# Kernel tuning notes

Measured on AMD Instinct MI355X. Metric: run time of the kernel, lower is better.

The kernel has to match this reference:

```python
import jax, jax.numpy as jnp
import numpy as np

N, D, K, E_T = 16384, 64, 3, 262144
EPS = 1e-8

def layernorm(x, g, b):
    m = x.mean(-1, keepdims=True)
    v = x.var(-1, keepdims=True)
    return (x - m) * jax.lax.rsqrt(v + 1e-5) * g + b

def knn_edges(coords, k):
    # PyG knn_graph(loop=False, flow='source_to_target'): edge (neighbor -> query)
    n = coords.shape[0]
    sq = jnp.sum(coords * coords, axis=-1)
    d = sq[:, None] + sq[None, :] - 2.0 * (coords @ coords.T)  # [N,N] sq dists
    d = d.at[jnp.arange(n), jnp.arange(n)].set(jnp.inf)  # exclude self
    _, idx = jax.lax.top_k(-d, k)  # [N,k] nearest neighbor indices
    src = idx.reshape(-1)
    dst = jnp.repeat(jnp.arange(n), k)
    return src, dst

def gcn_conv(x, W, b, src, dst, ew, n):
    h = x @ W
    deg = jax.ops.segment_sum(ew, dst, num_segments=n)
    dis = jnp.where(deg > 0, jax.lax.rsqrt(jnp.maximum(deg, EPS)), 0.0)
    norm = dis[src] * ew * dis[dst]
    out = jax.ops.segment_sum(h[src] * norm[:, None], dst, num_segments=n)
    return out + b

def setup_inputs():
    key = jax.random.key(0)
    ks = jax.random.split(key, 8)
    return {
        "sp_center_feat": jax.random.normal(ks[0], (N, D), jnp.float32),
        "edge_index_tran": jax.random.randint(ks[1], (2, E_T), 0, N),
        "edge_attr_rpe": jax.random.normal(ks[2], (E_T, 3), jnp.float32),
        "norm_index": jax.random.randint(ks[3], (2,), 0, N),
        "sp_crood": jax.random.uniform(ks[4], (N, 3), jnp.float32),
        "norm1_g": jnp.ones((D,), jnp.float32), "norm1_b": jnp.zeros((D,), jnp.float32),
        "norm2_g": jnp.ones((D,), jnp.float32), "norm2_b": jnp.zeros((D,), jnp.float32),
        "gcn_norm_g": jnp.ones((D,), jnp.float32), "gcn_norm_b": jnp.zeros((D,), jnp.float32),
        "W1": jax.random.normal(ks[5], (D, D), jnp.float32) / np.sqrt(D),
        "b1": jnp.zeros((D,), jnp.float32),
        "W2": jax.random.normal(ks[6], (D, D), jnp.float32) / np.sqrt(D),
        "b2": jnp.zeros((D,), jnp.float32),
    }

def reference(sp_center_feat, edge_index_tran, edge_attr_rpe, norm_index, sp_crood,
              norm1_g, norm1_b, norm2_g, norm2_b, gcn_norm_g, gcn_norm_b,
              W1, b1, W2, b2):
    n = sp_center_feat.shape[0]
    x = layernorm(sp_center_feat, norm1_g, norm1_b)
    x = x + x  # SPgrah (external transformer) stubbed as identity; module adds shortcut
    x = layernorm(x, norm2_g, norm2_b)
    shortcut = x
    src, dst = knn_edges(sp_crood, K)
    a = x[src]; b_ = x[dst]
    na = jnp.maximum(jnp.sqrt(jnp.sum(a * a, -1)), EPS)
    nb = jnp.maximum(jnp.sqrt(jnp.sum(b_ * b_, -1)), EPS)
    ew_knn = jax.nn.sigmoid(jnp.sum(a * b_, -1) / (na * nb))  # sigmoid(cosine sim)
    loop = jnp.arange(n)
    src2 = jnp.concatenate([src, loop])
    dst2 = jnp.concatenate([dst, loop])
    ew = jnp.concatenate([ew_knn, jnp.ones((n,), ew_knn.dtype)])  # self-loops w=1
    h = gcn_conv(x, W1, b1, src2, dst2, ew, n)
    h = jax.nn.relu(layernorm(h, gcn_norm_g, gcn_norm_b))
    h = gcn_conv(h, W2, b2, src2, dst2, ew, n)
    h = h + x  # residual inside SuperpointGCN
    return shortcut + h
```

## Files before the change

### kernel.cpp

```cpp
#include <hip/hip_runtime.h>
#include <math.h>

#define N 16384
#define GC 8
#define NCELL (GC*GC*GC)

__device__ __forceinline__ float wsum(float v){
  #pragma unroll
  for(int m=32;m>0;m>>=1) v += __shfl_xor(v,m,64);
  return v;
}

__device__ __forceinline__ void lexins(float dd,int j2,
    float&D0,float&D1,float&D2,int&I0,int&I1,int&I2){
  bool lt0=(dd<D0)||((dd==D0)&&(j2<I0));
  bool lt1=(dd<D1)||((dd==D1)&&(j2<I1));
  bool lt2=(dd<D2)||((dd==D2)&&(j2<I2));
  float nD2=lt1?D1:(lt2?dd:D2); int nI2=lt1?I1:(lt2?j2:I2);
  float nD1=lt0?D0:(lt1?dd:D1); int nI1=lt0?I0:(lt1?j2:I1);
  float nD0=lt0?dd:D0;          int nI0=lt0?j2:I0;
  D0=nD0;D1=nD1;D2=nD2;I0=nI0;I1=nI1;I2=nI2;
}

__device__ __forceinline__ float refdist(float qx,float qy,float qz,float qs,float4 cv){
  float dot=__fmaf_rn(qz,cv.z,__fmaf_rn(qy,cv.y,__fmul_rn(qx,cv.x)));
  float sc =__fadd_rn(qs,cv.w);
  return __fmaf_rn(-2.0f,dot,sc);
}

__global__ __launch_bounds__(256) void ln_kernel(const float* __restrict__ in,
    const float* __restrict__ g1,const float* __restrict__ b1,
    const float* __restrict__ g2,const float* __restrict__ b2,
    const float* __restrict__ coords,
    float* __restrict__ x, float* __restrict__ xn, float4* __restrict__ c4){
  int wave=threadIdx.x>>6, lane=threadIdx.x&63;
  int row=blockIdx.x*4+wave;
  float v=in[row*64+lane];
  float m=wsum(v)*(1.0f/64.0f);
  float d=v-m;
  float var=wsum(d*d)*(1.0f/64.0f);
  float y=d*(1.0f/sqrtf(var+1e-5f))*g1[lane]+b1[lane];
  y=y+y;
  float m2=wsum(y)*(1.0f/64.0f);
  float d2=y-m2;
  float var2=wsum(d2*d2)*(1.0f/64.0f);
  float z=d2*(1.0f/sqrtf(var2+1e-5f))*g2[lane]+b2[lane];
  x[row*64+lane]=z;
  float s=wsum(z*z);
  if(lane==0){
    xn[row]=fmaxf(sqrtf(s),1e-8f);
    float a=coords[row*3+0],b=coords[row*3+1],c=coords[row*3+2];
    float sq=__fadd_rn(__fadd_rn(__fmul_rn(a,a),__fmul_rn(b,b)),__fmul_rn(c,c));
    c4[row]=make_float4(a,b,c,sq);
  }
}

__global__ __launch_bounds__(1024) void prep(const float4* __restrict__ c4,
    float4* __restrict__ sc4, int* __restrict__ sidx, int* __restrict__ cellSt){
  __shared__ int cnt[NCELL];
  __shared__ int scanbuf[NCELL];
  int tid=threadIdx.x;
  if(tid<NCELL) cnt[tid]=0;
  __syncthreads();
  for(int i=tid;i<N;i+=1024){
    float4 v=c4[i];
    int cx=min(GC-1,(int)(v.x*(float)GC)), cy=min(GC-1,(int)(v.y*(float)GC)),
        cz=min(GC-1,(int)(v.z*(float)GC));
    atomicAdd(&cnt[(cz*GC+cy)*GC+cx],1);
  }
  __syncthreads();
  if(tid<NCELL) scanbuf[tid]=cnt[tid];
  __syncthreads();
  for(int off=1;off<NCELL;off<<=1){
    int t=0;
    if(tid>=off && tid<NCELL) t=scanbuf[tid-off];
    __syncthreads();
    if(tid<NCELL) scanbuf[tid]+=t;
    __syncthreads();
  }
  if(tid<NCELL){
    int excl=scanbuf[tid]-cnt[tid];
    cellSt[tid]=excl; cnt[tid]=excl;
    if(tid==NCELL-1) cellSt[NCELL]=scanbuf[NCELL-1];
  }
  __syncthreads();
  for(int i=tid;i<N;i+=1024){
    float4 v=c4[i];
    int cx=min(GC-1,(int)(v.x*(float)GC)), cy=min(GC-1,(int)(v.y*(float)GC)),
        cz=min(GC-1,(int)(v.z*(float)GC));
    int pos=atomicAdd(&cnt[(cz*GC+cy)*GC+cx],1);
    sc4[pos]=v; sidx[pos]=i;
  }
}

__global__ __launch_bounds__(256) void knn_ew(const float4* __restrict__ sc4,
    const int* __restrict__ sidx, const int* __restrict__ cellSt,
    const float4* __restrict__ c4, const float* __restrict__ x,
    const float* __restrict__ xn,
    int* __restrict__ knn, float* __restrict__ ew, float* __restrict__ dis){
  int tid=threadIdx.x, bid=blockIdx.x;
  int gt=bid*256+tid;
  int lane=tid&63;
  int slot=gt>>5, part=tid&31;

  float4 qv=sc4[slot]; int q=sidx[slot];
  float qx=qv.x,qy=qv.y,qz=qv.z,qs=qv.w;
  int cx=min(GC-1,(int)(qx*(float)GC)), cy=min(GC-1,(int)(qy*(float)GC)),
      cz=min(GC-1,(int)(qz*(float)GC));
  float D0=1e30f,D1=1e30f,D2=1e30f; int I0=0x7fffffff,I1=0x7fffffff,I2=0x7fffffff;
  int xlo=max(cx-1,0), xhi=min(cx+1,GC-1);
  const float cw=1.0f/(float)GC;
  float fy0=qy-(float)cy*cw, fy1=(float)(cy+1)*cw-qy;
  float fz0=qz-(float)cz*cw, fz1=(float)(cz+1)*cw-qz;
  const int OY[9]={0,-1,1, 0,0,-1, 1,-1,1};
  const int OZ[9]={0, 0,0,-1,1,-1,-1, 1,1};
  #pragma unroll 1
  for(int k=0;k<9;k++){
    int oy=OY[k], oz=OZ[k];
    int y2=cy+oy, z2=cz+oz;
    if(y2<0||y2>=GC||z2<0||z2>=GC) continue;
    if(k>0){
      float dy=(oy<0)?fy0:((oy>0)?fy1:0.0f);
      float dz=(oz<0)?fz0:((oz>0)?fz1:0.0f);
      float bnd=dy*dy+dz*dz;
      if(bnd>D2+1e-5f) continue;
    }
    int rowb=(z2*GC+y2)*GC;
    int p0=cellSt[rowb+xlo], p1=cellSt[rowb+xhi+1];
    for(int p=p0+part;p<p1;p+=32){
      float4 cv=sc4[p]; int j2=sidx[p];
      float dd=refdist(qx,qy,qz,qs,cv);
      dd=(j2==q)?1e30f:dd;
      lexins(dd,j2,D0,D1,D2,I0,I1,I2);
    }
  }
  #pragma unroll
  for(int m=1;m<32;m<<=1){
    float e0=__shfl_xor(D0,m),e1=__shfl_xor(D1,m),e2=__shfl_xor(D2,m);
    int   f0=__shfl_xor(I0,m),f1=__shfl_xor(I1,m),f2=__shfl_xor(I2,m);
    lexins(e0,f0,D0,D1,D2,I0,I1,I2);
    lexins(e1,f1,D0,D1,D2,I0,I1,I2);
    lexins(e2,f2,D0,D1,D2,I0,I1,I2);
  }
  bool flg=false;
  if(part==0){
    float mg=1e30f;
    mg=fminf(mg,(cx>0)?(qx-(float)(cx-1)*cw):1e30f);
    mg=fminf(mg,(cx<GC-1)?((float)(cx+2)*cw-qx):1e30f);
    mg=fminf(mg,(cy>0)?(qy-(float)(cy-1)*cw):1e30f);
    mg=fminf(mg,(cy<GC-1)?((float)(cy+2)*cw-qy):1e30f);
    mg=fminf(mg,(cz>0)?(qz-(float)(cz-1)*cw):1e30f);
    mg=fminf(mg,(cz<GC-1)?((float)(cz+2)*cw-qz):1e30f);
    float mg2=mg*mg*(1.0f-1e-5f);
    flg=!(D2<mg2);
  }
  unsigned long long mask=__ballot(flg);
  while(mask){
    int b=__ffsll((unsigned long long)mask)-1; mask&=mask-1;
    int qb=__shfl(q,b);
    float bx=__shfl(qx,b),by=__shfl(qy,b),bz=__shfl(qz,b),bs=__shfl(qs,b);
    float E0=1e30f,E1=1e30f,E2=1e30f; int F0=0x7fffffff,F1=0x7fffffff,F2=0x7fffffff;
    for(int j=lane;j<N;j+=64){
      float4 cv=c4[j];
      float dd=refdist(bx,by,bz,bs,cv);
      dd=(j==qb)?1e30f:dd;
      lexins(dd,j,E0,E1,E2,F0,F1,F2);
    }
    #pragma unroll
    for(int m=1;m<64;m<<=1){
      float e0=__shfl_xor(E0,m),e1=__shfl_xor(E1,m),e2=__shfl_xor(E2,m);
      int   f0=__shfl_xor(F0,m),f1=__shfl_xor(F1,m),f2=__shfl_xor(F2,m);
      lexins(e0,f0,E0,E1,E2,F0,F1,F2);
      lexins(e1,f1,E0,E1,E2,F0,F1,F2);
      lexins(e2,f2,E0,E1,E2,F0,F1,F2);
    }
    if(lane==b){ I0=F0; I1=F1; I2=F2; }
  }
  if(part==0){ knn[q*3+0]=I0; knn[q*3+1]=I1; knn[q*3+2]=I2; }

  for(int r=0;r<2;r++){
    int qi=__shfl(q,32*r);
    int s0=__shfl(I0,32*r), s1=__shfl(I1,32*r), s2=__shfl(I2,32*r);
    float xi=x[qi*64+lane];
    float xs0=x[s0*64+lane], xs1=x[s1*64+lane], xs2=x[s2*64+lane];
    float n0=xn[s0], n1=xn[s1], n2=xn[s2];
    float ni=xn[qi];
    float dt0=wsum(xs0*xi), dt1=wsum(xs1*xi), dt2=wsum(xs2*xi);
    float e0=1.f/(1.f+expf(-(dt0/(n0*ni))));
    float e1=1.f/(1.f+expf(-(dt1/(n1*ni))));
    float e2=1.f/(1.f+expf(-(dt2/(n2*ni))));
    if(lane==0){
      ew[qi*3+0]=e0; ew[qi*3+1]=e1; ew[qi*3+2]=e2;
      float ssum=((e0+e1)+e2);
      dis[qi]=1.f/sqrtf(ssum+1.0f);
    }
  }
}

__global__ __launch_bounds__(256) void agg1_w1(const float* __restrict__ x,
    const float* __restrict__ ew, const float* __restrict__ dis,
    const int* __restrict__ knn, const float* __restrict__ W1,
    const float* __restrict__ bb1, const float* __restrict__ gg,
    const float* __restrict__ gb, float* __restrict__ a1){
  __shared__ float rowbuf[4][64];
  int tid=threadIdx.x;
  int wave=tid>>6, lane=tid&63;
  float wcol[64];
  #pragma unroll
  for(int k=0;k<64;k++) wcol[k]=W1[k*64+lane];
  float bv=bb1[lane], gv=gg[lane], bv2=gb[lane];
  int nb=blockIdx.x*16+wave*4;
  for(int r=0;r<4;r++){
    int i=nb+r;
    float di=dis[i];
    float xa=x[i*64+lane]*(di*di);
    #pragma unroll
    for(int m=0;m<3;m++){
      int s=knn[i*3+m];
      xa+=x[s*64+lane]*(dis[s]*ew[i*3+m]*di);
    }
    rowbuf[wave][lane]=xa;
    const float4* rb=(const float4*)&rowbuf[wave][0];
    float acc=0.f;
    #pragma unroll
    for(int k4=0;k4<16;k4++){
      float4 av=rb[k4];
      acc=fmaf(av.x,wcol[k4*4+0],acc);
      acc=fmaf(av.y,wcol[k4*4+1],acc);
      acc=fmaf(av.z,wcol[k4*4+2],acc);
      acc=fmaf(av.w,wcol[k4*4+3],acc);
    }
    acc+=bv;
    float mu=wsum(acc)*(1.0f/64.0f);
    float dd=acc-mu;
    float var=wsum(dd*dd)*(1.0f/64.0f);
    float y=dd*(1.0f/sqrtf(var+1e-5f))*gv+bv2;
    a1[i*64+lane]=fmaxf(y,0.0f);
  }
}

__global__ __launch_bounds__(256) void agg2_w2(const float* __restrict__ a1,
    const float* __restrict__ ew, const float* __restrict__ dis,
    const int* __restrict__ knn, const float* __restrict__ W2,
    const float* __restrict__ bb2, const float* __restrict__ x,
    float* __restrict__ out){
  __shared__ float rowbuf[4][64];
  int tid=threadIdx.x;
  int wave=tid>>6, lane=tid&63;
  float wcol[64];
  #pragma unroll
  for(int k=0;k<64;k++) wcol[k]=W2[k*64+lane];
  float bv=bb2[lane];
  int nb=blockIdx.x*16+wave*4;
  for(int r=0;r<4;r++){
    int i=nb+r;
    float di=dis[i];
    float aa=a1[i*64+lane]*(di*di);
    #pragma unroll
    for(int m=0;m<3;m++){
      int s=knn[i*3+m];
      aa+=a1[s*64+lane]*(dis[s]*ew[i*3+m]*di);
    }
    rowbuf[wave][lane]=aa;
    const float4* rb=(const float4*)&rowbuf[wave][0];
    float acc=0.f;
    #pragma unroll
    for(int k4=0;k4<16;k4++){
      float4 av=rb[k4];
      acc=fmaf(av.x,wcol[k4*4+0],acc);
      acc=fmaf(av.y,wcol[k4*4+1],acc);
      acc=fmaf(av.z,wcol[k4*4+2],acc);
      acc=fmaf(av.w,wcol[k4*4+3],acc);
    }
    acc+=bv;
    float xv=x[i*64+lane];
    out[i*64+lane]=(acc+xv)+xv;
  }
}

extern "C" void kernel_launch(void* const* d_in, const int* in_sizes, int n_in,
                              void* d_out, int out_size, void* d_ws, size_t ws_size,
                              hipStream_t stream){
  const float* feat  =(const float*)d_in[0];
  const float* coords=(const float*)d_in[4];
  const float* g1 =(const float*)d_in[5];
  const float* b1n=(const float*)d_in[6];
  const float* g2 =(const float*)d_in[7];
  const float* b2n=(const float*)d_in[8];
  const float* gg =(const float*)d_in[9];
  const float* gb =(const float*)d_in[10];
  const float* W1 =(const float*)d_in[11];
  const float* bb1=(const float*)d_in[12];
  const float* W2 =(const float*)d_in[13];
  const float* bb2=(const float*)d_in[14];
  float* out=(float*)d_out;

  char* ws=(char*)d_ws;
  size_t o=0;
  float*  x      =(float*) (ws+o); o+=(size_t)N*64*4;
  float*  a1     =(float*) (ws+o); o+=(size_t)N*64*4;
  float*  xn     =(float*) (ws+o); o+=(size_t)N*4;
  float*  ew     =(float*) (ws+o); o+=(size_t)N*3*4;
  float*  dis    =(float*) (ws+o); o+=(size_t)N*4;
  int*    knn    =(int*)   (ws+o); o+=(size_t)N*3*4;
  float4* c4     =(float4*)(ws+o); o+=(size_t)N*16;
  float4* sc4    =(float4*)(ws+o); o+=(size_t)N*16;
  int*    sidx   =(int*)   (ws+o); o+=(size_t)N*4;
  int*    cellSt =(int*)   (ws+o); o+=(size_t)(NCELL+1)*4;
  (void)ws_size; (void)in_sizes; (void)n_in; (void)out_size;

  hipLaunchKernelGGL(ln_kernel, dim3(N/4),  dim3(256),  0, stream, feat,g1,b1n,g2,b2n,coords,x,xn,c4);
  hipLaunchKernelGGL(prep,      dim3(1),    dim3(1024), 0, stream, c4,sc4,sidx,cellSt);
  hipLaunchKernelGGL(knn_ew,    dim3(2048), dim3(256),  0, stream, sc4,sidx,cellSt,c4,x,xn,knn,ew,dis);
  hipLaunchKernelGGL(agg1_w1,   dim3(N/16), dim3(256),  0, stream, x,ew,dis,knn,W1,bb1,gg,gb,a1);
  hipLaunchKernelGGL(agg2_w2,   dim3(N/16), dim3(256),  0, stream, a1,ew,dis,knn,W2,bb2,x,out);
}
```

Measured before the change: 169.1 us.

## Parallelize grid binning across blocks and software-prefetch gather rows in aggregation

The single-block prep kernel is removed. Cell counting moves into the layernorm kernel as global atomics, and a new 64-block scatter kernel has each block redundantly scan the 512 cell counts, then place points using a global cursor. This takes the serial one-CU binning stage off the critical path, at the cost of a memset and global atomic contention. Separately, both aggregation kernels now prefetch the next row's neighbor gathers into registers while the current row's matvec runs. This hides gather latency but raises register pressure. Within-cell point order becomes nondeterministic, which can alter kNN tie-breaking only through sorted order.

```diff
diff --git a/kernel.cpp b/kernel.cpp
--- a/kernel.cpp
+++ b/kernel.cpp
@@ -32,7 +32,8 @@
     const float* __restrict__ g1,const float* __restrict__ b1,
     const float* __restrict__ g2,const float* __restrict__ b2,
     const float* __restrict__ coords,
-    float* __restrict__ x, float* __restrict__ xn, float4* __restrict__ c4){
+    float* __restrict__ x, float* __restrict__ xn, float4* __restrict__ c4,
+    int* __restrict__ cnt){
   int wave=threadIdx.x>>6, lane=threadIdx.x&63;
   int row=blockIdx.x*4+wave;
   float v=in[row*64+lane];
@@ -52,45 +53,43 @@
     float a=coords[row*3+0],b=coords[row*3+1],c=coords[row*3+2];
     float sq=__fadd_rn(__fadd_rn(__fmul_rn(a,a),__fmul_rn(b,b)),__fmul_rn(c,c));
     c4[row]=make_float4(a,b,c,sq);
-  }
-}
-
-__global__ __launch_bounds__(1024) void prep(const float4* __restrict__ c4,
+    int cx=min(GC-1,(int)(a*(float)GC)), cy=min(GC-1,(int)(b*(float)GC)),
+        cz=min(GC-1,(int)(c*(float)GC));
+    atomicAdd(&cnt[(cz*GC+cy)*GC+cx],1);
+  }
+}
+
+__global__ __launch_bounds__(256) void scatter_k(const float4* __restrict__ c4,
+    const int* __restrict__ cnt, int* __restrict__ cursor,
     float4* __restrict__ sc4, int* __restrict__ sidx, int* __restrict__ cellSt){
-  __shared__ int cnt[NCELL];
-  __shared__ int scanbuf[NCELL];
+  __shared__ int buf[NCELL];
   int tid=threadIdx.x;
-  if(tid<NCELL) cnt[tid]=0;
+  int c0v=cnt[tid], c1v=cnt[tid+256];
+  buf[tid]=c0v; buf[tid+256]=c1v;
   __syncthreads();
-  for(int i=tid;i<N;i+=1024){
-    float4 v=c4[i];
-    int cx=min(GC-1,(int)(v.x*(float)GC)), cy=min(GC-1,(int)(v.y*(float)GC)),
-        cz=min(GC-1,(int)(v.z*(float)GC));
-    atomicAdd(&cnt[(cz*GC+cy)*GC+cx],1);
+  #pragma unroll
+  for(int off=1;off<NCELL;off<<=1){
+    int v0=(tid>=off)?buf[tid-off]:0;
+    int v1=(tid+256>=off)?buf[tid+256-off]:0;
+    __syncthreads();
+    buf[tid]+=v0; buf[tid+256]+=v1;
+    __syncthreads();
+  }
+  int e0=buf[tid]-c0v, e1=buf[tid+256]-c1v;
+  if(blockIdx.x==0){
+    cellSt[tid]=e0; cellSt[tid+256]=e1;
+    if(tid==0) cellSt[NCELL]=N;
   }
   __syncthreads();
-  if(tid<NCELL) scanbuf[tid]=cnt[tid];
+  buf[tid]=e0; buf[tid+256]=e1;
   __syncthreads();
-  for(int off=1;off<NCELL;off<<=1){
-    int t=0;
-    if(tid>=off && tid<NCELL) t=scanbuf[tid-off];
-    __syncthreads();
-    if(tid<NCELL) scanbuf[tid]+=t;
-    __syncthreads();
-  }
-  if(tid<NCELL){
-    int excl=scanbuf[tid]-cnt[tid];
-    cellSt[tid]=excl; cnt[tid]=excl;
-    if(tid==NCELL-1) cellSt[NCELL]=scanbuf[NCELL-1];
-  }
-  __syncthreads();
-  for(int i=tid;i<N;i+=1024){
-    float4 v=c4[i];
-    int cx=min(GC-1,(int)(v.x*(float)GC)), cy=min(GC-1,(int)(v.y*(float)GC)),
-        cz=min(GC-1,(int)(v.z*(float)GC));
-    int pos=atomicAdd(&cnt[(cz*GC+cy)*GC+cx],1);
-    sc4[pos]=v; sidx[pos]=i;
-  }
+  int i=blockIdx.x*256+tid;
+  float4 v=c4[i];
+  int cx=min(GC-1,(int)(v.x*(float)GC)), cy=min(GC-1,(int)(v.y*(float)GC)),
+      cz=min(GC-1,(int)(v.z*(float)GC));
+  int cell=(cz*GC+cy)*GC+cx;
+  int pos=buf[cell]+atomicAdd(&cursor[cell],1);
+  sc4[pos]=v; sidx[pos]=i;
 }
 
 __global__ __launch_bounds__(256) void knn_ew(const float4* __restrict__ sc4,
@@ -210,15 +209,28 @@
   for(int k=0;k<64;k++) wcol[k]=W1[k*64+lane];
   float bv=bb1[lane], gv=gg[lane], bv2=gb[lane];
   int nb=blockIdx.x*16+wave*4;
+  float xrA,dAA,xsA0,xsA1,xsA2,wA0,wA1,wA2;
+  float xrB,dBB,xsB0,xsB1,xsB2,wB0,wB1,wB2;
+  {
+    int i=nb;
+    float di=dis[i]; dAA=di*di;
+    xrA=x[i*64+lane];
+    int s0=knn[i*3+0], s1=knn[i*3+1], s2=knn[i*3+2];
+    xsA0=x[s0*64+lane]; xsA1=x[s1*64+lane]; xsA2=x[s2*64+lane];
+    wA0=dis[s0]*ew[i*3+0]*di; wA1=dis[s1]*ew[i*3+1]*di; wA2=dis[s2]*ew[i*3+2]*di;
+  }
+  #pragma unroll
   for(int r=0;r<4;r++){
-    int i=nb+r;
-    float di=dis[i];
-    float xa=x[i*64+lane]*(di*di);
-    #pragma unroll
-    for(int m=0;m<3;m++){
-      int s=knn[i*3+m];
-      xa+=x[s*64+lane]*(dis[s]*ew[i*3+m]*di);
-    }
+    if(r<3){
+      int i=nb+r+1;
+      float di=dis[i]; dBB=di*di;
+      xrB=x[i*64+lane];
+      int s0=knn[i*3+0], s1=knn[i*3+1], s2=knn[i*3+2];
+      xsB0=x[s0*64+lane]; xsB1=x[s1*64+lane]; xsB2=x[s2*64+lane];
+      wB0=dis[s0]*ew[i*3+0]*di; wB1=dis[s1]*ew[i*3+1]*di; wB2=dis[s2]*ew[i*3+2]*di;
+    }
+    float xa=xrA*dAA;
+    xa=fmaf(xsA0,wA0,xa); xa=fmaf(xsA1,wA1,xa); xa=fmaf(xsA2,wA2,xa);
     rowbuf[wave][lane]=xa;
     const float4* rb=(const float4*)&rowbuf[wave][0];
     float acc=0.f;
@@ -235,7 +247,10 @@
     float dd=acc-mu;
     float var=wsum(dd*dd)*(1.0f/64.0f);
     float y=dd*(1.0f/sqrtf(var+1e-5f))*gv+bv2;
-    a1[i*64+lane]=fmaxf(y,0.0f);
+    a1[(nb+r)*64+lane]=fmaxf(y,0.0f);
+    xrA=xrB; dAA=dBB;
+    xsA0=xsB0; xsA1=xsB1; xsA2=xsB2;
+    wA0=wB0; wA1=wB1; wA2=wB2;
   }
 }
 
@@ -252,15 +267,28 @@
   for(int k=0;k<64;k++) wcol[k]=W2[k*64+lane];
   float bv=bb2[lane];
   int nb=blockIdx.x*16+wave*4;
+  float xrA,dAA,xsA0,xsA1,xsA2,wA0,wA1,wA2;
+  float xrB,dBB,xsB0,xsB1,xsB2,wB0,wB1,wB2;
+  {
+    int i=nb;
+    float di=dis[i]; dAA=di*di;
+    xrA=a1[i*64+lane];
+    int s0=knn[i*3+0], s1=knn[i*3+1], s2=knn[i*3+2];
+    xsA0=a1[s0*64+lane]; xsA1=a1[s1*64+lane]; xsA2=a1[s2*64+lane];
+    wA0=dis[s0]*ew[i*3+0]*di; wA1=dis[s1]*ew[i*3+1]*di; wA2=dis[s2]*ew[i*3+2]*di;
+  }
+  #pragma unroll
   for(int r=0;r<4;r++){
-    int i=nb+r;
-    float di=dis[i];
-    float aa=a1[i*64+lane]*(di*di);
-    #pragma unroll
-    for(int m=0;m<3;m++){
-      int s=knn[i*3+m];
-      aa+=a1[s*64+lane]*(dis[s]*ew[i*3+m]*di);
-    }
+    if(r<3){
+      int i=nb+r+1;
+      float di=dis[i]; dBB=di*di;
+      xrB=a1[i*64+lane];
+      int s0=knn[i*3+0], s1=knn[i*3+1], s2=knn[i*3+2];
+      xsB0=a1[s0*64+lane]; xsB1=a1[s1*64+lane]; xsB2=a1[s2*64+lane];
+      wB0=dis[s0]*ew[i*3+0]*di; wB1=dis[s1]*ew[i*3+1]*di; wB2=dis[s2]*ew[i*3+2]*di;
+    }
+    float aa=xrA*dAA;
+    aa=fmaf(xsA0,wA0,aa); aa=fmaf(xsA1,wA1,aa); aa=fmaf(xsA2,wA2,aa);
     rowbuf[wave][lane]=aa;
     const float4* rb=(const float4*)&rowbuf[wave][0];
     float acc=0.f;
@@ -273,8 +301,11 @@
       acc=fmaf(av.w,wcol[k4*4+3],acc);
     }
     acc+=bv;
-    float xv=x[i*64+lane];
-    out[i*64+lane]=(acc+xv)+xv;
+    float xv=x[(nb+r)*64+lane];
+    out[(nb+r)*64+lane]=(acc+xv)+xv;
+    xrA=xrB; dAA=dBB;
+    xsA0=xsB0; xsA1=xsB1; xsA2=xsB2;
+    wA0=wB0; wA1=wB1; wA2=wB2;
   }
 }
 
@@ -307,11 +338,15 @@
   float4* sc4    =(float4*)(ws+o); o+=(size_t)N*16;
   int*    sidx   =(int*)   (ws+o); o+=(size_t)N*4;
   int*    cellSt =(int*)   (ws+o); o+=(size_t)(NCELL+1)*4;
+  o=(o+255)&~(size_t)255;
+  int*    cnt    =(int*)   (ws+o); o+=(size_t)NCELL*4;
+  int*    cursor =(int*)   (ws+o); o+=(size_t)NCELL*4;
   (void)ws_size; (void)in_sizes; (void)n_in; (void)out_size;
 
-  hipLaunchKernelGGL(ln_kernel, dim3(N/4),  dim3(256),  0, stream, feat,g1,b1n,g2,b2n,coords,x,xn,c4);
-  hipLaunchKernelGGL(prep,      dim3(1),    dim3(1024), 0, stream, c4,sc4,sidx,cellSt);
-  hipLaunchKernelGGL(knn_ew,    dim3(2048), dim3(256),  0, stream, sc4,sidx,cellSt,c4,x,xn,knn,ew,dis);
-  hipLaunchKernelGGL(agg1_w1,   dim3(N/16), dim3(256),  0, stream, x,ew,dis,knn,W1,bb1,gg,gb,a1);
-  hipLaunchKernelGGL(agg2_w2,   dim3(N/16), dim3(256),  0, stream, a1,ew,dis,knn,W2,bb2,x,out);
-}
+  hipMemsetAsync((void*)cnt, 0, (size_t)2*NCELL*4, stream);
+  hipLaunchKernelGGL(ln_kernel, dim3(N/4),   dim3(256), 0, stream, feat,g1,b1n,g2,b2n,coords,x,xn,c4,cnt);
+  hipLaunchKernelGGL(scatter_k, dim3(N/256), dim3(256), 0, stream, c4,cnt,cursor,sc4,sidx,cellSt);
+  hipLaunchKernelGGL(knn_ew,    dim3(2048),  dim3(256), 0, stream, sc4,sidx,cellSt,c4,x,xn,knn,ew,dis);
+  hipLaunchKernelGGL(agg1_w1,   dim3(N/16),  dim3(256), 0, stream, x,ew,dis,knn,W1,bb1,gg,gb,a1);
+  hipLaunchKernelGGL(agg2_w2,   dim3(N/16),  dim3(256), 0, stream, a1,ew,dis,knn,W2,bb2,x,out);
+}
```

Measured after the change: 155.4 us. -8.1%, faster.
